# Kernel tuning notes

Measured on AMD Instinct MI355X. Metric: run time of the kernel, lower is better.

Reference implementation:

```python
import jax, jax.numpy as jnp
import numpy as np

DT = 0.05
DELAY = int(1.0 / DT)  # 20 steps of synaptic delay
NUM_ASCS = 2
R_MEM = 0.1     # membrane resistance
SIGMA_V = 1.0   # sigmoid smoothing of spiking nonlinearity
V_RESET = 0.0

B, T, IN, HID, OUT = 64, 200, 512, 1024, 512


def setup_inputs() -> dict:
    key = jax.random.key(0)
    ks = jax.random.split(key, 10)
    return {
        "x": jax.random.normal(ks[0], (B, T, IN), dtype=jnp.float32),
        "W_in": jax.random.normal(ks[1], (IN, HID), dtype=jnp.float32) / np.sqrt(IN),
        "W_lat": jax.random.normal(ks[2], (HID, HID), dtype=jnp.float32) / np.sqrt(HID),
        "thresh": jax.random.normal(ks[3], (1, HID), dtype=jnp.float32) * 0.1,
        "trans_k_m": jax.random.normal(ks[4], (1, HID), dtype=jnp.float32) * 0.1,
        "trans_asc_k": jax.random.normal(ks[5], (NUM_ASCS, 1, HID), dtype=jnp.float32) * 0.1,
        "asc_amp": jax.random.normal(ks[6], (NUM_ASCS, 1, HID), dtype=jnp.float32) * 0.1,
        "trans_asc_r": jax.random.normal(ks[7], (NUM_ASCS, 1, HID), dtype=jnp.float32) * 0.1,
        "W_out": jax.random.normal(ks[8], (OUT, HID), dtype=jnp.float32) / np.sqrt(HID),
        "b_out": jax.random.normal(ks[9], (OUT,), dtype=jnp.float32) * 0.01,
    }


def _glifr_rnn(x, W_in, W_lat, thresh, trans_k_m, trans_asc_k, asc_amp, trans_asc_r, W_out, b_out):
    Bx, Tx, _ = x.shape
    H = W_lat.shape[0]
    # rate transforms keep dt*k in (0,1); r in (-1,1)
    k_m = jax.nn.sigmoid(trans_k_m) / DT          # [1,H]
    k_asc = jax.nn.sigmoid(trans_asc_k) / DT      # [A,1,H]
    asc_r = 1.0 - 2.0 * jax.nn.sigmoid(trans_asc_r)
    # precompute input projection for all timesteps: [T,B,H]
    x_proj = jnp.swapaxes(jnp.einsum("bti,ih->bth", x, W_in), 0, 1)

    def step(carry, xp):
        firing, voltage, asc, buf = carry
        firing_delayed = buf[0]                       # firing DELAY steps ago
        syn = xp + firing_delayed @ W_lat             # synaptic current [B,H]
        asc_new = (asc_amp + asc_r * asc) * firing * (DT * k_asc) + (1.0 - DT * k_asc) * asc
        volt_new = (R_MEM * DT * k_m) * (syn + asc_new.sum(0)) \
                   + (1.0 - DT * k_m) * voltage + DT * k_m * V_RESET
        firing_new = jax.nn.sigmoid((volt_new - thresh) / SIGMA_V)
        buf_new = jnp.concatenate([buf[1:], firing_new[None]], axis=0)
        out = firing_new @ W_out.T + b_out            # per-step linear readout
        return (firing_new, volt_new, asc_new, buf_new), out

    z = jnp.zeros((Bx, H), dtype=x.dtype)
    carry0 = (z, z, jnp.zeros((NUM_ASCS, Bx, H), x.dtype), jnp.zeros((DELAY, Bx, H), x.dtype))
    _, outs = jax.lax.scan(step, carry0, x_proj)      # outs: [T,B,OUT]
    return jnp.swapaxes(outs, 0, 1)                   # [B,T,OUT]


def reference(x, W_in, W_lat, thresh, trans_k_m, trans_asc_k, asc_amp, trans_asc_r, W_out, b_out):
    return _glifr_rnn(x, W_in, W_lat, thresh, trans_k_m, trans_asc_k, asc_amp, trans_asc_r, W_out, b_out)
```

## Files before the change

kernel.cpp:

```cpp
#include <hip/hip_runtime.h>


typedef float f32x4 __attribute__((ext_vector_type(4)));
typedef __bf16 bf16x8 __attribute__((ext_vector_type(8)));
typedef unsigned short ushortx8 __attribute__((ext_vector_type(8)));
typedef unsigned short ushortx4 __attribute__((ext_vector_type(4)));

__device__ __forceinline__ unsigned short f2b(float f) {
    unsigned int u = __float_as_uint(f);
    unsigned int r = u + 0x7FFFu + ((u >> 16) & 1u);
    return (unsigned short)(r >> 16);
}
__device__ __forceinline__ float sigmoidf(float x) {
    return 1.0f / (1.0f + __expf(-x));
}

__device__ __forceinline__ void gl_lds16(const unsigned short* g, unsigned short* l) {
    __builtin_amdgcn_global_load_lds(
        (const __attribute__((address_space(1))) void*)g,
        (__attribute__((address_space(3))) void*)l, 16, 0, 0);
}

__global__ __launch_bounds__(256) void transpose_f32_to_bf16(
    const float* __restrict__ in, unsigned short* __restrict__ out,
    int R, int C)
{
    __shared__ unsigned short t[64][65];
    int bx = blockIdx.x * 64, by = blockIdx.y * 64;
    int tx = threadIdx.x & 63, ty = threadIdx.x >> 6;
    for (int r = ty; r < 64; r += 4)
        t[r][tx] = f2b(in[(size_t)(by + r) * C + bx + tx]);
    __syncthreads();
    for (int r = ty; r < 64; r += 4)
        out[(size_t)(bx + r) * R + by + tx] = t[tx][r];
}

__global__ __launch_bounds__(256) void convert_f32_to_bf16(
    const float* __restrict__ in, unsigned short* __restrict__ out)
{
    int i = (blockIdx.x * 256 + threadIdx.x) * 4;
    f32x4 v = *(const f32x4*)(in + i);
    ushortx4 o;
    o[0] = f2b(v[0]); o[1] = f2b(v[1]); o[2] = f2b(v[2]); o[3] = f2b(v[3]);
    *(ushortx4*)(out + i) = o;
}

__global__ __launch_bounds__(256) void convert_x(
    const float* __restrict__ x, unsigned short* __restrict__ xb)
{
    size_t i8 = (size_t)(blockIdx.x * 256 + threadIdx.x) * 8;
    int m = (int)(i8 >> 9), k = (int)(i8 & 511);
    int b = m & 63, t = m >> 6;
    const float* src = x + ((size_t)b * 200 + t) * 512 + k;
    f32x4 v0 = *(const f32x4*)src;
    f32x4 v1 = *(const f32x4*)(src + 4);
    ushortx8 o;
    o[0] = f2b(v0[0]); o[1] = f2b(v0[1]); o[2] = f2b(v0[2]); o[3] = f2b(v0[3]);
    o[4] = f2b(v1[0]); o[5] = f2b(v1[1]); o[6] = f2b(v1[2]); o[7] = f2b(v1[3]);
    *(ushortx8*)(xb + i8) = o;
}

template<int BM, int BN, int MODE>
__global__ __launch_bounds__(256) void gemm_nt(
    const unsigned short* __restrict__ A,
    const unsigned short* __restrict__ Bt,
    float* __restrict__ outf,
    const float* __restrict__ bias,
    int M, int N, int K)
{
    constexpr int WM = BM / 2, WN = BN / 2;
    constexpr int TM = WM / 16, TN = WN / 16;

    __shared__ unsigned short Asm[BM * 64];
    __shared__ unsigned short Bsm[BN * 64];

    const int tid  = threadIdx.x;
    const int wave = tid >> 6, lane = tid & 63;
    const int m16  = lane & 15, quad = lane >> 4;
    const int bm0  = blockIdx.y * BM, bn0 = blockIdx.x * BN;
    const int wr   = (wave >> 1) * WM, wc = (wave & 1) * WN;
    const int sr   = lane >> 3;
    const int sc   = lane & 7;

    f32x4 acc[TM][TN];
#pragma unroll
    for (int i = 0; i < TM; i++)
#pragma unroll
        for (int j = 0; j < TN; j++)
            acc[i][j] = (f32x4){0.f, 0.f, 0.f, 0.f};

    for (int k0 = 0; k0 < K; k0 += 64) {
#pragma unroll
        for (int g = wave; g < BM / 8; g += 4) {
            int r = g * 8 + sr;
            int c = sc ^ (r & 7);
            gl_lds16(A + (size_t)(bm0 + r) * K + k0 + c * 8, Asm + g * 512);
        }
#pragma unroll
        for (int g = wave; g < BN / 8; g += 4) {
            int r = g * 8 + sr;
            int c = sc ^ (r & 7);
            gl_lds16(Bt + (size_t)(bn0 + r) * K + k0 + c * 8, Bsm + g * 512);
        }
        __syncthreads();

        ushortx8 af[2][TM], bfr[2][TN];
#pragma unroll
        for (int kh = 0; kh < 2; kh++) {
#pragma unroll
            for (int i = 0; i < TM; i++) {
                int ra = wr + i * 16 + m16;
                af[kh][i] = *(const ushortx8*)(
                    Asm + ra * 64 + (((kh * 4 + quad) ^ (ra & 7)) * 8));
            }
#pragma unroll
            for (int j = 0; j < TN; j++) {
                int rb = wc + j * 16 + m16;
                bfr[kh][j] = *(const ushortx8*)(
                    Bsm + rb * 64 + (((kh * 4 + quad) ^ (rb & 7)) * 8));
            }
        }
#pragma unroll
        for (int i = 0; i < TM; i++)
#pragma unroll
            for (int j = 0; j < TN; j++) {
                acc[i][j] = __builtin_amdgcn_mfma_f32_16x16x32_bf16(
                    __builtin_bit_cast(bf16x8, af[0][i]),
                    __builtin_bit_cast(bf16x8, bfr[0][j]),
                    acc[i][j], 0, 0, 0);
                acc[i][j] = __builtin_amdgcn_mfma_f32_16x16x32_bf16(
                    __builtin_bit_cast(bf16x8, af[1][i]),
                    __builtin_bit_cast(bf16x8, bfr[1][j]),
                    acc[i][j], 0, 0, 0);
            }
        __syncthreads();
    }

#pragma unroll
    for (int i = 0; i < TM; i++)
#pragma unroll
        for (int j = 0; j < TN; j++) {
            int col = bn0 + wc + j * 16 + m16;
            float bv = (MODE == 2) ? bias[col] : 0.f;
#pragma unroll
            for (int v = 0; v < 4; v++) {
                int row = bm0 + wr + i * 16 + quad * 4 + v;
                if (MODE == 2) {
                    size_t o = (size_t)((row & 63) * 200 + (row >> 6)) * N + col;
                    outf[o] = acc[i][j][v] + bv;
                } else {
                    outf[(size_t)row * N + col] = acc[i][j][v];
                }
            }
        }
}

__global__ __launch_bounds__(256) void fused_chunk(
    const unsigned short* __restrict__ Fprev,
    const unsigned short* __restrict__ Wlat,
    const float* __restrict__ xproj,
    float* __restrict__ state,
    unsigned short* __restrict__ Fc,
    const float* __restrict__ thresh,
    const float* __restrict__ t_km,
    const float* __restrict__ t_ak,
    const float* __restrict__ amp,
    const float* __restrict__ t_ar)
{
    const int BH = 64 * 1024;
    __shared__ __align__(16) char lds[21120];
    unsigned short* Asm = (unsigned short*)lds;
    unsigned short* Bsm = (unsigned short*)(lds + 10240);
    float* synT = (float*)lds;

    const int tid  = threadIdx.x;
    const int wave = tid >> 6, lane = tid & 63;
    const int m16  = lane & 15, quad = lane >> 4;
    const int sr   = lane >> 3, sc = lane & 7;
    const int b0   = blockIdx.y * 4, h0 = blockIdx.x * 64;
    const int wrow = (wave >> 1) * 48;
    const int wc   = (wave & 1) * 32;

    f32x4 acc[3][2];
#pragma unroll
    for (int i = 0; i < 3; i++) {
        if (i < 2 || wave < 2) {
#pragma unroll
            for (int j = 0; j < 2; j++)
#pragma unroll
                for (int v = 0; v < 4; v++) {
                    int row = wrow + i * 16 + quad * 4 + v;
                    int col = h0 + wc + j * 16 + m16;
                    acc[i][j][v] = xproj[(size_t)(((row >> 2) << 6) + b0 + (row & 3)) * 1024 + col];
                }
        }
    }

    for (int k0 = 0; k0 < 1024; k0 += 64) {
        for (int g = wave; g < 10; g += 4) {
            int r = g * 8 + sr;
            int c = sc ^ (r & 7);
            int m = ((r >> 2) << 6) + b0 + (r & 3);
            gl_lds16(Fprev + (size_t)m * 1024 + k0 + c * 8, Asm + g * 512);
        }
        for (int g = wave; g < 8; g += 4) {
            int r = g * 8 + sr;
            int c = sc ^ (r & 7);
            gl_lds16(Wlat + (size_t)(h0 + r) * 1024 + k0 + c * 8, Bsm + g * 512);
        }
        __syncthreads();

        ushortx8 af[2][3], bfr[2][2];
#pragma unroll
        for (int kh = 0; kh < 2; kh++) {
#pragma unroll
            for (int i = 0; i < 3; i++) {
                if (i < 2 || wave < 2) {
                    int ra = wrow + i * 16 + m16;
                    af[kh][i] = *(const ushortx8*)(
                        Asm + ra * 64 + (((kh * 4 + quad) ^ (ra & 7)) * 8));
                }
            }
#pragma unroll
            for (int j = 0; j < 2; j++) {
                int rb = wc + j * 16 + m16;
                bfr[kh][j] = *(const ushortx8*)(
                    Bsm + rb * 64 + (((kh * 4 + quad) ^ (rb & 7)) * 8));
            }
        }
#pragma unroll
        for (int i = 0; i < 3; i++) {
            if (i < 2 || wave < 2) {
#pragma unroll
                for (int j = 0; j < 2; j++) {
                    acc[i][j] = __builtin_amdgcn_mfma_f32_16x16x32_bf16(
                        __builtin_bit_cast(bf16x8, af[0][i]),
                        __builtin_bit_cast(bf16x8, bfr[0][j]), acc[i][j], 0, 0, 0);
                    acc[i][j] = __builtin_amdgcn_mfma_f32_16x16x32_bf16(
                        __builtin_bit_cast(bf16x8, af[1][i]),
                        __builtin_bit_cast(bf16x8, bfr[1][j]), acc[i][j], 0, 0, 0);
                }
            }
        }
        __syncthreads();
    }

#pragma unroll
    for (int i = 0; i < 3; i++) {
        if (i < 2 || wave < 2) {
#pragma unroll
            for (int j = 0; j < 2; j++)
#pragma unroll
                for (int v = 0; v < 4; v++) {
                    int row = wrow + i * 16 + quad * 4 + v;
                    synT[row * 66 + wc + j * 16 + m16] = acc[i][j][v];
                }
        }
    }
    __syncthreads();

    const int h    = h0 + lane;
    const int gidx = (b0 + wave) * 1024 + h;
    float th  = thresh[h];
    float sm  = sigmoidf(t_km[h]);
    float rm  = 0.1f * sm;
    float om  = 1.0f - sm;
    float sa0 = sigmoidf(t_ak[h]);
    float sa1 = sigmoidf(t_ak[1024 + h]);
    float am0 = amp[h];
    float am1 = amp[1024 + h];
    float r0  = 1.0f - 2.0f * sigmoidf(t_ar[h]);
    float r1  = 1.0f - 2.0f * sigmoidf(t_ar[1024 + h]);

    float volt = state[gidx];
    float a0   = state[BH + gidx];
    float a1   = state[2 * BH + gidx];
    float fir  = state[3 * BH + gidx];

#pragma unroll
    for (int s = 0; s < 20; s++) {
        float sv  = synT[(s * 4 + wave) * 66 + lane];
        float na0 = (am0 + r0 * a0) * fir * sa0 + (1.f - sa0) * a0;
        float na1 = (am1 + r1 * a1) * fir * sa1 + (1.f - sa1) * a1;
        volt = rm * (sv + na0 + na1) + om * volt;
        fir  = sigmoidf(volt - th);
        Fc[(size_t)s * BH + gidx] = f2b(fir);
        a0 = na0; a1 = na1;
    }
    state[gidx]          = volt;
    state[BH + gidx]     = a0;
    state[2 * BH + gidx] = a1;
    state[3 * BH + gidx] = fir;
}

__global__ __launch_bounds__(256) void chunk_step(
    const float* __restrict__ syn,
    float* __restrict__ state,
    unsigned short* __restrict__ F,
    const float* __restrict__ thresh,
    const float* __restrict__ t_km,
    const float* __restrict__ t_ak,
    const float* __restrict__ amp,
    const float* __restrict__ t_ar)
{
    const int BH = 64 * 1024;
    int idx = blockIdx.x * 256 + threadIdx.x;
    int h = idx & 1023;

    float th  = thresh[h];
    float sm  = sigmoidf(t_km[h]);
    float rm  = 0.1f * sm;
    float om  = 1.0f - sm;
    float sa0 = sigmoidf(t_ak[h]);
    float sa1 = sigmoidf(t_ak[1024 + h]);
    float am0 = amp[h];
    float am1 = amp[1024 + h];
    float r0  = 1.0f - 2.0f * sigmoidf(t_ar[h]);
    float r1  = 1.0f - 2.0f * sigmoidf(t_ar[1024 + h]);

    float volt = 0.f, a0 = 0.f, a1 = 0.f, fir = 0.f;

#pragma unroll
    for (int s = 0; s < 20; s++) {
        float sv  = syn[(size_t)s * BH + idx];
        float na0 = (am0 + r0 * a0) * fir * sa0 + (1.f - sa0) * a0;
        float na1 = (am1 + r1 * a1) * fir * sa1 + (1.f - sa1) * a1;
        volt = rm * (sv + na0 + na1) + om * volt;
        fir  = sigmoidf(volt - th);
        F[(size_t)s * BH + idx] = f2b(fir);
        a0 = na0; a1 = na1;
    }
    state[idx]          = volt;
    state[BH + idx]     = a0;
    state[2 * BH + idx] = a1;
    state[3 * BH + idx] = fir;
}

extern "C" void kernel_launch(void* const* d_in, const int* in_sizes, int n_in,
                              void* d_out, int out_size, void* d_ws, size_t ws_size,
                              hipStream_t stream)
{
    const float* x      = (const float*)d_in[0];
    const float* W_in   = (const float*)d_in[1];
    const float* W_lat  = (const float*)d_in[2];
    const float* thresh = (const float*)d_in[3];
    const float* t_km   = (const float*)d_in[4];
    const float* t_ak   = (const float*)d_in[5];
    const float* amp    = (const float*)d_in[6];
    const float* t_ar   = (const float*)d_in[7];
    const float* W_out  = (const float*)d_in[8];
    const float* b_out  = (const float*)d_in[9];
    float* out = (float*)d_out;

    char* ws = (char*)d_ws;
    float*          syn   = (float*)ws;
    float*          state = (float*)(ws + 52428800);
    unsigned short* F     = (unsigned short*)(ws + 53477376);
    unsigned short* xb    = F;
    unsigned short* WinT  = (unsigned short*)(ws + 79691776);
    unsigned short* WlatT = (unsigned short*)(ws + 80740352);
    unsigned short* WoutB = (unsigned short*)(ws + 82837504);

    transpose_f32_to_bf16<<<dim3(16, 8),  256, 0, stream>>>(W_in,  WinT,  512,  1024);
    transpose_f32_to_bf16<<<dim3(16, 16), 256, 0, stream>>>(W_lat, WlatT, 1024, 1024);
    convert_f32_to_bf16<<<512, 256, 0, stream>>>(W_out, WoutB);
    convert_x<<<3200, 256, 0, stream>>>(x, xb);

    gemm_nt<128, 128, 0><<<dim3(1024 / 128, 12800 / 128), 256, 0, stream>>>(
        xb, WinT, syn, nullptr, 12800, 1024, 512);

    chunk_step<<<256, 256, 0, stream>>>(syn, state, F, thresh, t_km, t_ak, amp, t_ar);

    const size_t CHUNK = 20 * 64 * 1024;
    for (int c = 1; c < 10; c++) {
        fused_chunk<<<dim3(16, 16), 256, 0, stream>>>(
            F + (size_t)(c - 1) * CHUNK, WlatT,
            syn + (size_t)c * CHUNK, state, F + (size_t)c * CHUNK,
            thresh, t_km, t_ak, amp, t_ar);
    }

    gemm_nt<128, 128, 2><<<dim3(512 / 128, 12800 / 128), 256, 0, stream>>>(
        F, WoutB, out, b_out, 12800, 512, 1024);
}
```

Before: 302.8 us.

## Replace per-chunk launches with one cooperative persistent kernel and double-buffered LDS

Merges the initial chunk_step and the nine fused_chunk launches into a single cooperative kernel that loops over chunks, using grid.sync between them. Neuron state stays in registers instead of round-tripping through a global state buffer. The K-loop also double-buffers the LDS staging so the next tile's loads overlap with the current MFMAs. This trades kernel-launch gaps and state traffic for grid-wide barrier cost, and needs all 256 blocks to be co-resident.

```diff
diff --git a/kernel.cpp b/kernel.cpp
--- a/kernel.cpp
+++ b/kernel.cpp
@@ -1,4 +1,7 @@
 #include <hip/hip_runtime.h>
+#include <hip/hip_cooperative_groups.h>
+
+namespace cg = cooperative_groups;
 
 
 typedef float f32x4 __attribute__((ext_vector_type(4)));
@@ -155,12 +158,10 @@
         }
 }
 
-__global__ __launch_bounds__(256) void fused_chunk(
-    const unsigned short* __restrict__ Fprev,
+__global__ __launch_bounds__(256) void chunk_chain(
     const unsigned short* __restrict__ Wlat,
     const float* __restrict__ xproj,
-    float* __restrict__ state,
-    unsigned short* __restrict__ Fc,
+    unsigned short* __restrict__ F,
     const float* __restrict__ thresh,
     const float* __restrict__ t_km,
     const float* __restrict__ t_ak,
@@ -168,96 +169,22 @@
     const float* __restrict__ t_ar)
 {
     const int BH = 64 * 1024;
-    __shared__ __align__(16) char lds[21120];
-    unsigned short* Asm = (unsigned short*)lds;
-    unsigned short* Bsm = (unsigned short*)(lds + 10240);
+    const size_t CHUNK = 20 * 64 * 1024;
+    __shared__ __align__(16) char lds[36864];
+    unsigned short* Ab[2] = {(unsigned short*)lds,
+                             (unsigned short*)(lds + 10240)};
+    unsigned short* Bb[2] = {(unsigned short*)(lds + 20480),
+                             (unsigned short*)(lds + 28672)};
     float* synT = (float*)lds;
 
     const int tid  = threadIdx.x;
     const int wave = tid >> 6, lane = tid & 63;
     const int m16  = lane & 15, quad = lane >> 4;
     const int sr   = lane >> 3, sc = lane & 7;
-    const int b0   = blockIdx.y * 4, h0 = blockIdx.x * 64;
+    const int bx   = blockIdx.x;
+    const int h0   = (bx & 15) * 64, b0 = (bx >> 4) * 4;
     const int wrow = (wave >> 1) * 48;
     const int wc   = (wave & 1) * 32;
-
-    f32x4 acc[3][2];
-#pragma unroll
-    for (int i = 0; i < 3; i++) {
-        if (i < 2 || wave < 2) {
-#pragma unroll
-            for (int j = 0; j < 2; j++)
-#pragma unroll
-                for (int v = 0; v < 4; v++) {
-                    int row = wrow + i * 16 + quad * 4 + v;
-                    int col = h0 + wc + j * 16 + m16;
-                    acc[i][j][v] = xproj[(size_t)(((row >> 2) << 6) + b0 + (row & 3)) * 1024 + col];
-                }
-        }
-    }
-
-    for (int k0 = 0; k0 < 1024; k0 += 64) {
-        for (int g = wave; g < 10; g += 4) {
-            int r = g * 8 + sr;
-            int c = sc ^ (r & 7);
-            int m = ((r >> 2) << 6) + b0 + (r & 3);
-            gl_lds16(Fprev + (size_t)m * 1024 + k0 + c * 8, Asm + g * 512);
-        }
-        for (int g = wave; g < 8; g += 4) {
-            int r = g * 8 + sr;
-            int c = sc ^ (r & 7);
-            gl_lds16(Wlat + (size_t)(h0 + r) * 1024 + k0 + c * 8, Bsm + g * 512);
-        }
-        __syncthreads();
-
-        ushortx8 af[2][3], bfr[2][2];
-#pragma unroll
-        for (int kh = 0; kh < 2; kh++) {
-#pragma unroll
-            for (int i = 0; i < 3; i++) {
-                if (i < 2 || wave < 2) {
-                    int ra = wrow + i * 16 + m16;
-                    af[kh][i] = *(const ushortx8*)(
-                        Asm + ra * 64 + (((kh * 4 + quad) ^ (ra & 7)) * 8));
-                }
-            }
-#pragma unroll
-            for (int j = 0; j < 2; j++) {
-                int rb = wc + j * 16 + m16;
-                bfr[kh][j] = *(const ushortx8*)(
-                    Bsm + rb * 64 + (((kh * 4 + quad) ^ (rb & 7)) * 8));
-            }
-        }
-#pragma unroll
-        for (int i = 0; i < 3; i++) {
-            if (i < 2 || wave < 2) {
-#pragma unroll
-                for (int j = 0; j < 2; j++) {
-                    acc[i][j] = __builtin_amdgcn_mfma_f32_16x16x32_bf16(
-                        __builtin_bit_cast(bf16x8, af[0][i]),
-                        __builtin_bit_cast(bf16x8, bfr[0][j]), acc[i][j], 0, 0, 0);
-                    acc[i][j] = __builtin_amdgcn_mfma_f32_16x16x32_bf16(
-                        __builtin_bit_cast(bf16x8, af[1][i]),
-                        __builtin_bit_cast(bf16x8, bfr[1][j]), acc[i][j], 0, 0, 0);
-                }
-            }
-        }
-        __syncthreads();
-    }
-
-#pragma unroll
-    for (int i = 0; i < 3; i++) {
-        if (i < 2 || wave < 2) {
-#pragma unroll
-            for (int j = 0; j < 2; j++)
-#pragma unroll
-                for (int v = 0; v < 4; v++) {
-                    int row = wrow + i * 16 + quad * 4 + v;
-                    synT[row * 66 + wc + j * 16 + m16] = acc[i][j][v];
-                }
-        }
-    }
-    __syncthreads();
 
     const int h    = h0 + lane;
     const int gidx = (b0 + wave) * 1024 + h;
@@ -272,68 +199,130 @@
     float r0  = 1.0f - 2.0f * sigmoidf(t_ar[h]);
     float r1  = 1.0f - 2.0f * sigmoidf(t_ar[1024 + h]);
 
-    float volt = state[gidx];
-    float a0   = state[BH + gidx];
-    float a1   = state[2 * BH + gidx];
-    float fir  = state[3 * BH + gidx];
+    float volt = 0.f, a0 = 0.f, a1 = 0.f, fir = 0.f;
+
+    cg::grid_group grid = cg::this_grid();
 
 #pragma unroll
     for (int s = 0; s < 20; s++) {
-        float sv  = synT[(s * 4 + wave) * 66 + lane];
+        float sv  = xproj[(size_t)(s * 64 + b0 + wave) * 1024 + h];
         float na0 = (am0 + r0 * a0) * fir * sa0 + (1.f - sa0) * a0;
         float na1 = (am1 + r1 * a1) * fir * sa1 + (1.f - sa1) * a1;
         volt = rm * (sv + na0 + na1) + om * volt;
         fir  = sigmoidf(volt - th);
-        Fc[(size_t)s * BH + gidx] = f2b(fir);
+        F[(size_t)s * BH + gidx] = f2b(fir);
         a0 = na0; a1 = na1;
     }
-    state[gidx]          = volt;
-    state[BH + gidx]     = a0;
-    state[2 * BH + gidx] = a1;
-    state[3 * BH + gidx] = fir;
-}
-
-__global__ __launch_bounds__(256) void chunk_step(
-    const float* __restrict__ syn,
-    float* __restrict__ state,
-    unsigned short* __restrict__ F,
-    const float* __restrict__ thresh,
-    const float* __restrict__ t_km,
-    const float* __restrict__ t_ak,
-    const float* __restrict__ amp,
-    const float* __restrict__ t_ar)
-{
-    const int BH = 64 * 1024;
-    int idx = blockIdx.x * 256 + threadIdx.x;
-    int h = idx & 1023;
-
-    float th  = thresh[h];
-    float sm  = sigmoidf(t_km[h]);
-    float rm  = 0.1f * sm;
-    float om  = 1.0f - sm;
-    float sa0 = sigmoidf(t_ak[h]);
-    float sa1 = sigmoidf(t_ak[1024 + h]);
-    float am0 = amp[h];
-    float am1 = amp[1024 + h];
-    float r0  = 1.0f - 2.0f * sigmoidf(t_ar[h]);
-    float r1  = 1.0f - 2.0f * sigmoidf(t_ar[1024 + h]);
-
-    float volt = 0.f, a0 = 0.f, a1 = 0.f, fir = 0.f;
-
-#pragma unroll
-    for (int s = 0; s < 20; s++) {
-        float sv  = syn[(size_t)s * BH + idx];
-        float na0 = (am0 + r0 * a0) * fir * sa0 + (1.f - sa0) * a0;
-        float na1 = (am1 + r1 * a1) * fir * sa1 + (1.f - sa1) * a1;
-        volt = rm * (sv + na0 + na1) + om * volt;
-        fir  = sigmoidf(volt - th);
-        F[(size_t)s * BH + idx] = f2b(fir);
-        a0 = na0; a1 = na1;
+    __threadfence();
+    grid.sync();
+
+    for (int c = 1; c < 10; c++) {
+        const unsigned short* Fprev = F + (size_t)(c - 1) * CHUNK;
+        const float* xp = xproj + (size_t)c * CHUNK;
+        unsigned short* Fc = F + (size_t)c * CHUNK;
+
+        f32x4 acc[3][2];
+#pragma unroll
+        for (int i = 0; i < 3; i++) {
+            if (i < 2 || wave < 2) {
+#pragma unroll
+                for (int j = 0; j < 2; j++)
+#pragma unroll
+                    for (int v = 0; v < 4; v++) {
+                        int row = wrow + i * 16 + quad * 4 + v;
+                        int col = h0 + wc + j * 16 + m16;
+                        acc[i][j][v] =
+                            xp[(size_t)(((row >> 2) << 6) + b0 + (row & 3)) * 1024 + col];
+                    }
+            }
+        }
+
+        auto STAGE = [&](unsigned short* Abuf, unsigned short* Bbuf, int k0) {
+            for (int g = wave; g < 10; g += 4) {
+                int r = g * 8 + sr;
+                int cc = sc ^ (r & 7);
+                int m = ((r >> 2) << 6) + b0 + (r & 3);
+                gl_lds16(Fprev + (size_t)m * 1024 + k0 + cc * 8, Abuf + g * 512);
+            }
+            for (int g = wave; g < 8; g += 4) {
+                int r = g * 8 + sr;
+                int cc = sc ^ (r & 7);
+                gl_lds16(Wlat + (size_t)(h0 + r) * 1024 + k0 + cc * 8, Bbuf + g * 512);
+            }
+        };
+        auto COMPUTE = [&](const unsigned short* Abuf, const unsigned short* Bbuf) {
+            ushortx8 af[2][3], bfr[2][2];
+#pragma unroll
+            for (int kh = 0; kh < 2; kh++) {
+#pragma unroll
+                for (int i = 0; i < 3; i++) {
+                    if (i < 2 || wave < 2) {
+                        int ra = wrow + i * 16 + m16;
+                        af[kh][i] = *(const ushortx8*)(
+                            Abuf + ra * 64 + (((kh * 4 + quad) ^ (ra & 7)) * 8));
+                    }
+                }
+#pragma unroll
+                for (int j = 0; j < 2; j++) {
+                    int rb = wc + j * 16 + m16;
+                    bfr[kh][j] = *(const ushortx8*)(
+                        Bbuf + rb * 64 + (((kh * 4 + quad) ^ (rb & 7)) * 8));
+                }
+            }
+#pragma unroll
+            for (int i = 0; i < 3; i++) {
+                if (i < 2 || wave < 2) {
+#pragma unroll
+                    for (int j = 0; j < 2; j++) {
+                        acc[i][j] = __builtin_amdgcn_mfma_f32_16x16x32_bf16(
+                            __builtin_bit_cast(bf16x8, af[0][i]),
+                            __builtin_bit_cast(bf16x8, bfr[0][j]), acc[i][j], 0, 0, 0);
+                        acc[i][j] = __builtin_amdgcn_mfma_f32_16x16x32_bf16(
+                            __builtin_bit_cast(bf16x8, af[1][i]),
+                            __builtin_bit_cast(bf16x8, bfr[1][j]), acc[i][j], 0, 0, 0);
+                    }
+                }
+            }
+        };
+
+        STAGE(Ab[0], Bb[0], 0);
+        __syncthreads();
+        for (int k = 0; k < 16; k += 2) {
+            STAGE(Ab[1], Bb[1], (k + 1) * 64);
+            COMPUTE(Ab[0], Bb[0]);
+            __syncthreads();
+            if (k + 2 < 16) STAGE(Ab[0], Bb[0], (k + 2) * 64);
+            COMPUTE(Ab[1], Bb[1]);
+            __syncthreads();
+        }
+
+#pragma unroll
+        for (int i = 0; i < 3; i++) {
+            if (i < 2 || wave < 2) {
+#pragma unroll
+                for (int j = 0; j < 2; j++)
+#pragma unroll
+                    for (int v = 0; v < 4; v++) {
+                        int row = wrow + i * 16 + quad * 4 + v;
+                        synT[row * 66 + wc + j * 16 + m16] = acc[i][j][v];
+                    }
+            }
+        }
+        __syncthreads();
+
+#pragma unroll
+        for (int s = 0; s < 20; s++) {
+            float sv  = synT[(s * 4 + wave) * 66 + lane];
+            float na0 = (am0 + r0 * a0) * fir * sa0 + (1.f - sa0) * a0;
+            float na1 = (am1 + r1 * a1) * fir * sa1 + (1.f - sa1) * a1;
+            volt = rm * (sv + na0 + na1) + om * volt;
+            fir  = sigmoidf(volt - th);
+            Fc[(size_t)s * BH + gidx] = f2b(fir);
+            a0 = na0; a1 = na1;
+        }
+        __threadfence();
+        if (c < 9) grid.sync();
     }
-    state[idx]          = volt;
-    state[BH + idx]     = a0;
-    state[2 * BH + idx] = a1;
-    state[3 * BH + idx] = fir;
 }
 
 extern "C" void kernel_launch(void* const* d_in, const int* in_sizes, int n_in,
@@ -354,7 +343,6 @@
 
     char* ws = (char*)d_ws;
     float*          syn   = (float*)ws;
-    float*          state = (float*)(ws + 52428800);
     unsigned short* F     = (unsigned short*)(ws + 53477376);
     unsigned short* xb    = F;
     unsigned short* WinT  = (unsigned short*)(ws + 79691776);
@@ -369,15 +357,11 @@
     gemm_nt<128, 128, 0><<<dim3(1024 / 128, 12800 / 128), 256, 0, stream>>>(
         xb, WinT, syn, nullptr, 12800, 1024, 512);
 
-    chunk_step<<<256, 256, 0, stream>>>(syn, state, F, thresh, t_km, t_ak, amp, t_ar);
-
-    const size_t CHUNK = 20 * 64 * 1024;
-    for (int c = 1; c < 10; c++) {
-        fused_chunk<<<dim3(16, 16), 256, 0, stream>>>(
-            F + (size_t)(c - 1) * CHUNK, WlatT,
-            syn + (size_t)c * CHUNK, state, F + (size_t)c * CHUNK,
-            thresh, t_km, t_ak, amp, t_ar);
-    }
+    void* args[] = {(void*)&WlatT, (void*)&syn, (void*)&F,
+                    (void*)&thresh, (void*)&t_km, (void*)&t_ak,
+                    (void*)&amp, (void*)&t_ar};
+    hipLaunchCooperativeKernel((const void*)chunk_chain,
+                               dim3(256), dim3(256), args, 0, stream);
 
     gemm_nt<128, 128, 2><<<dim3(512 / 128, 12800 / 128), 256, 0, stream>>>(
         F, WoutB, out, b_out, 12800, 512, 1024);
```

After: 747.1 us. 147% more time.

## Overlap output readout GEMM with recurrent chunk kernels via extra blocks

Applied to the files above, without the earlier changes.

The output projection for chunk c-1 is now computed by 160 extra blocks appended to each fused_chunk launch, which read the previous chunk's firing buffer that is already complete. The recurrent blocks are unchanged and only used 256 blocks, so the readout work can run on otherwise idle compute units instead of in a separate full-size GEMM at the end. Only the last chunk's readout remains as a small standalone GEMM. The cost is extra work inside each serialized chunk launch, which could lengthen the critical path if the readout blocks compete with the recurrent blocks for CUs or bandwidth.

```diff
diff --git a/kernel.cpp b/kernel.cpp
--- a/kernel.cpp
+++ b/kernel.cpp
@@ -66,7 +66,7 @@
     const unsigned short* __restrict__ Bt,
     float* __restrict__ outf,
     const float* __restrict__ bias,
-    int M, int N, int K)
+    int M, int N, int K, int t_base)
 {
     constexpr int WM = BM / 2, WN = BN / 2;
     constexpr int TM = WM / 16, TN = WN / 16;
@@ -146,7 +146,7 @@
             for (int v = 0; v < 4; v++) {
                 int row = bm0 + wr + i * 16 + quad * 4 + v;
                 if (MODE == 2) {
-                    size_t o = (size_t)((row & 63) * 200 + (row >> 6)) * N + col;
+                    size_t o = (size_t)((row & 63) * 200 + t_base + (row >> 6)) * N + col;
                     outf[o] = acc[i][j][v] + bv;
                 } else {
                     outf[(size_t)row * N + col] = acc[i][j][v];
@@ -161,23 +161,106 @@
     const float* __restrict__ xproj,
     float* __restrict__ state,
     unsigned short* __restrict__ Fc,
+    const unsigned short* __restrict__ WoutB,
+    float* __restrict__ out,
+    const float* __restrict__ b_out,
     const float* __restrict__ thresh,
     const float* __restrict__ t_km,
     const float* __restrict__ t_ak,
     const float* __restrict__ amp,
-    const float* __restrict__ t_ar)
+    const float* __restrict__ t_ar,
+    int t_base_prev)
 {
     const int BH = 64 * 1024;
     __shared__ __align__(16) char lds[21120];
-    unsigned short* Asm = (unsigned short*)lds;
-    unsigned short* Bsm = (unsigned short*)(lds + 10240);
-    float* synT = (float*)lds;
 
     const int tid  = threadIdx.x;
     const int wave = tid >> 6, lane = tid & 63;
     const int m16  = lane & 15, quad = lane >> 4;
     const int sr   = lane >> 3, sc = lane & 7;
-    const int b0   = blockIdx.y * 4, h0 = blockIdx.x * 64;
+    const int bx   = blockIdx.x;
+
+    if (bx >= 256) {
+        unsigned short* Asm = (unsigned short*)lds;
+        unsigned short* Bsm = (unsigned short*)(lds + 8192);
+        const int rb  = bx - 256;
+        const int bn0 = (rb & 7) * 64;
+        const int bm0 = (rb >> 3) * 64;
+        const int wr  = (wave >> 1) * 32, wc = (wave & 1) * 32;
+
+        f32x4 acc[2][2];
+#pragma unroll
+        for (int i = 0; i < 2; i++)
+#pragma unroll
+            for (int j = 0; j < 2; j++)
+                acc[i][j] = (f32x4){0.f, 0.f, 0.f, 0.f};
+
+        for (int k0 = 0; k0 < 1024; k0 += 64) {
+#pragma unroll
+            for (int g = wave; g < 8; g += 4) {
+                int r = g * 8 + sr;
+                int c = sc ^ (r & 7);
+                gl_lds16(Fprev + (size_t)(bm0 + r) * 1024 + k0 + c * 8, Asm + g * 512);
+            }
+#pragma unroll
+            for (int g = wave; g < 8; g += 4) {
+                int r = g * 8 + sr;
+                int c = sc ^ (r & 7);
+                gl_lds16(WoutB + (size_t)(bn0 + r) * 1024 + k0 + c * 8, Bsm + g * 512);
+            }
+            __syncthreads();
+
+            ushortx8 af[2][2], bfr[2][2];
+#pragma unroll
+            for (int kh = 0; kh < 2; kh++) {
+#pragma unroll
+                for (int i = 0; i < 2; i++) {
+                    int ra = wr + i * 16 + m16;
+                    af[kh][i] = *(const ushortx8*)(
+                        Asm + ra * 64 + (((kh * 4 + quad) ^ (ra & 7)) * 8));
+                }
+#pragma unroll
+                for (int j = 0; j < 2; j++) {
+                    int rbr = wc + j * 16 + m16;
+                    bfr[kh][j] = *(const ushortx8*)(
+                        Bsm + rbr * 64 + (((kh * 4 + quad) ^ (rbr & 7)) * 8));
+                }
+            }
+#pragma unroll
+            for (int i = 0; i < 2; i++)
+#pragma unroll
+                for (int j = 0; j < 2; j++) {
+                    acc[i][j] = __builtin_amdgcn_mfma_f32_16x16x32_bf16(
+                        __builtin_bit_cast(bf16x8, af[0][i]),
+                        __builtin_bit_cast(bf16x8, bfr[0][j]), acc[i][j], 0, 0, 0);
+                    acc[i][j] = __builtin_amdgcn_mfma_f32_16x16x32_bf16(
+                        __builtin_bit_cast(bf16x8, af[1][i]),
+                        __builtin_bit_cast(bf16x8, bfr[1][j]), acc[i][j], 0, 0, 0);
+                }
+            __syncthreads();
+        }
+
+#pragma unroll
+        for (int i = 0; i < 2; i++)
+#pragma unroll
+            for (int j = 0; j < 2; j++) {
+                int col = bn0 + wc + j * 16 + m16;
+                float bv = b_out[col];
+#pragma unroll
+                for (int v = 0; v < 4; v++) {
+                    int row = bm0 + wr + i * 16 + quad * 4 + v;
+                    size_t o = (size_t)((row & 63) * 200 + t_base_prev + (row >> 6)) * 512 + col;
+                    out[o] = acc[i][j][v] + bv;
+                }
+            }
+        return;
+    }
+
+    unsigned short* Asm = (unsigned short*)lds;
+    unsigned short* Bsm = (unsigned short*)(lds + 10240);
+    float* synT = (float*)lds;
+
+    const int b0   = (bx >> 4) * 4, h0 = (bx & 15) * 64;
     const int wrow = (wave >> 1) * 48;
     const int wc   = (wave & 1) * 32;
 
@@ -223,9 +306,9 @@
             }
 #pragma unroll
             for (int j = 0; j < 2; j++) {
-                int rb = wc + j * 16 + m16;
+                int rbr = wc + j * 16 + m16;
                 bfr[kh][j] = *(const ushortx8*)(
-                    Bsm + rb * 64 + (((kh * 4 + quad) ^ (rb & 7)) * 8));
+                    Bsm + rbr * 64 + (((kh * 4 + quad) ^ (rbr & 7)) * 8));
             }
         }
 #pragma unroll
@@ -367,18 +450,19 @@
     convert_x<<<3200, 256, 0, stream>>>(x, xb);
 
     gemm_nt<128, 128, 0><<<dim3(1024 / 128, 12800 / 128), 256, 0, stream>>>(
-        xb, WinT, syn, nullptr, 12800, 1024, 512);
+        xb, WinT, syn, nullptr, 12800, 1024, 512, 0);
 
     chunk_step<<<256, 256, 0, stream>>>(syn, state, F, thresh, t_km, t_ak, amp, t_ar);
 
     const size_t CHUNK = 20 * 64 * 1024;
     for (int c = 1; c < 10; c++) {
-        fused_chunk<<<dim3(16, 16), 256, 0, stream>>>(
+        fused_chunk<<<dim3(416), 256, 0, stream>>>(
             F + (size_t)(c - 1) * CHUNK, WlatT,
             syn + (size_t)c * CHUNK, state, F + (size_t)c * CHUNK,
-            thresh, t_km, t_ak, amp, t_ar);
-    }
-
-    gemm_nt<128, 128, 2><<<dim3(512 / 128, 12800 / 128), 256, 0, stream>>>(
-        F, WoutB, out, b_out, 12800, 512, 1024);
-}
+            WoutB, out, b_out,
+            thresh, t_km, t_ak, amp, t_ar, (c - 1) * 20);
+    }
+
+    gemm_nt<128, 128, 2><<<dim3(512 / 128, 1280 / 128), 256, 0, stream>>>(
+        F + (size_t)9 * CHUNK, WoutB, out, b_out, 1280, 512, 1024, 180);
+}
```

Measured after the change: 307.9 us. Within noise of the previous version (+1.7%).
